# Optimization experiments

Hardware: AMD Instinct MI355X
Metric: run time of the kernel (lower is better)

## Reference

```python
import jax, jax.numpy as jnp
import numpy as np

N = 50000
E = 800000
D_IN = 128
D_OUT = 128
LN_EPS = 1e-5
NEG_SLOPE = 0.01  # torch LeakyReLU default


def setup_inputs() -> dict:
    key = jax.random.key(0)
    ks = jax.random.split(key, 6)
    x = jax.random.normal(ks[0], (N, D_IN), dtype=jnp.float32)
    edgeIndex = jax.random.randint(ks[1], (2, E), 0, N, dtype=jnp.int64)
    edgeAttribute = jax.random.uniform(ks[2], (E,), dtype=jnp.float32)
    ln_w = jnp.ones((D_IN,), jnp.float32)
    ln_b = jnp.zeros((D_IN,), jnp.float32)
    W_gcn = jax.random.normal(ks[3], (D_IN, D_OUT), dtype=jnp.float32) / np.sqrt(D_IN)
    b_gcn = jnp.zeros((D_OUT,), jnp.float32)
    W_lin = jax.random.normal(ks[4], (D_IN, D_OUT), dtype=jnp.float32) / np.sqrt(D_IN)
    b_lin = jnp.zeros((D_OUT,), jnp.float32)
    return dict(x=x, edgeIndex=edgeIndex, edgeAttribute=edgeAttribute,
                ln_w=ln_w, ln_b=ln_b, W_gcn=W_gcn, b_gcn=b_gcn,
                W_lin=W_lin, b_lin=b_lin)


def _layernorm(x, w, b):
    mu = jnp.mean(x, axis=-1, keepdims=True)
    var = jnp.mean(jnp.square(x - mu), axis=-1, keepdims=True)
    return (x - mu) * jax.lax.rsqrt(var + LN_EPS) * w + b


def _gcn_conv(x, edge_index, edge_weight, W, b):
    # PyG GCNConv: h = X W; add self-loops (w=1); D^-1/2 (A+I) D^-1/2 h + b
    n = x.shape[0]
    h = x @ W  # [N, D_OUT]
    loop = jnp.arange(n, dtype=edge_index.dtype)
    row = jnp.concatenate([edge_index[0], loop])  # source j
    col = jnp.concatenate([edge_index[1], loop])  # target i
    ew = jnp.concatenate([edge_weight, jnp.ones((n,), edge_weight.dtype)])
    deg = jax.ops.segment_sum(ew, col, num_segments=n)  # in-degree (weighted)
    dinv = jnp.where(deg > 0, jax.lax.rsqrt(deg), 0.0)
    norm = dinv[row] * ew * dinv[col]  # [E+N]
    msg = h[row] * norm[:, None]  # gather-scale, [E+N, D_OUT]
    out = jax.ops.segment_sum(msg, col, num_segments=n)  # scatter-add
    return out + b


def reference(x, edgeIndex, edgeAttribute, ln_w, ln_b, W_gcn, b_gcn, W_lin, b_lin):
    xn = _layernorm(x, ln_w, ln_b)
    g = _gcn_conv(xn, edgeIndex, edgeAttribute, W_gcn, b_gcn)
    x_out = jnp.where(g >= 0, g, NEG_SLOPE * g)  # LeakyReLU; dropout in eval = identity
    x_trans = xn @ W_lin + b_lin
    return x_out + x_trans
```

## Files before the change

kernel.cpp:

```cpp
#include <hip/hip_runtime.h>
#include <hip/hip_bf16.h>

#define DD 128
#define LN_EPS_ 1e-5f
#define SLOPE 0.01f
#define SB 128
#define NB 391
#define HB 64
#define LNB 12500

typedef __attribute__((ext_vector_type(8))) short bf16x8;
typedef __attribute__((ext_vector_type(4))) float f32x4;
typedef __attribute__((ext_vector_type(2))) float f32x2;
typedef __attribute__((ext_vector_type(2))) unsigned int u32x2;

__device__ __forceinline__ __hip_bfloat162 pack_bf162(float a, float b) {
  __hip_bfloat162 r;
  r.x = __float2bfloat16(a);
  r.y = __float2bfloat16(b);
  return r;
}

__device__ __forceinline__ float b2f(short v) {
  return __uint_as_float(((unsigned)(unsigned short)v) << 16);
}

__device__ __forceinline__ unsigned short f2bbits(float f) {
  __hip_bfloat16 h = __float2bfloat16(f);
  return *(unsigned short*)&h;
}


__launch_bounds__(256)
__global__ void k_big1(const int* __restrict__ eic, int* __restrict__ bhistT,
                       int* __restrict__ bcurOff,
                       const float* __restrict__ x, const float* __restrict__ lnw,
                       const float* __restrict__ lnb, __hip_bfloat162* __restrict__ xnB,
                       const float* __restrict__ Wg, const float* __restrict__ Wl,
                       __hip_bfloat16* __restrict__ pw, int ne, int n) {
  __shared__ int lh[NB];
  int bid = blockIdx.x;
  int t = threadIdx.x;
  if (bid < HB) {
    for (int i = t; i < NB; i += 256) lh[i] = 0;
    __syncthreads();
    for (int e = bid * 256 + t; e < ne; e += HB * 256) atomicAdd(&lh[eic[e] >> 7], 1);
    __syncthreads();
    for (int i = t; i < NB; i += 256) bhistT[i * HB + bid] = lh[i];
    if (bid == 0)
      for (int i = t; i < NB; i += 256) bcurOff[i] = 0;
  } else if (bid < HB + LNB) {
    int lane = t & 63;
    int row = (bid - HB) * 4 + (t >> 6);
    if (row >= n) return;
    float2 v = ((const float2*)(x + (size_t)row * DD))[lane];
    float s = v.x + v.y;
#pragma unroll
    for (int m = 32; m; m >>= 1) s += __shfl_xor(s, m, 64);
    float mu = s * 0.0078125f;
    float ex = v.x - mu, ey = v.y - mu;
    float q = ex * ex + ey * ey;
#pragma unroll
    for (int m = 32; m; m >>= 1) q += __shfl_xor(q, m, 64);
    float rstd = rsqrtf(q * 0.0078125f + LN_EPS_);
    float2 wv = ((const float2*)lnw)[lane];
    float2 bv = ((const float2*)lnb)[lane];
    xnB[(size_t)row * 64 + lane] =
        pack_bf162(ex * rstd * wv.x + bv.x, ey * rstd * wv.y + bv.y);
  } else {
    int idx = (bid - HB - LNB) * 256 + t;
    if (idx >= 2 * 16384) return;
    int j = idx & 7;
    int lane = (idx >> 3) & 63;
    int ks = (idx >> 9) & 3;
    int ct = (idx >> 11) & 7;
    int mat = idx >> 14;
    int col = ct * 16 + (lane & 15);
    int k = ks * 32 + (lane >> 4) * 8 + j;
    const float* W = mat ? Wl : Wg;
    pw[idx] = __float2bfloat16(W[k * DD + col]);
  }
}


__launch_bounds__(512)
__global__ void k_scatterA(const int* __restrict__ ei, const float* __restrict__ ew,
                           const int* __restrict__ bhistT, int* __restrict__ bcurOff,
                           int* __restrict__ bbase, uint2* __restrict__ packA, int ne) {
  __shared__ int lhist[NB];
  __shared__ int lbase[NB];
  __shared__ int sc[2][512];
  int t = threadIdx.x;

  int v = 0;
  if (t < NB) {
    const int4* col = (const int4*)(bhistT + t * HB);
#pragma unroll
    for (int b = 0; b < HB / 4; ++b) {
      int4 c = col[b];
      v += c.x + c.y + c.z + c.w;
    }
  }
  sc[0][t] = v;
  __syncthreads();
  int pb = 0;
  for (int off = 1; off < 512; off <<= 1) {
    sc[pb ^ 1][t] = sc[pb][t] + (t >= off ? sc[pb][t - off] : 0);
    pb ^= 1;
    __syncthreads();
  }
  int inc = sc[pb][t];
  if (t < NB) {
    lbase[t] = inc - v;
    lhist[t] = 0;
  }
  if (blockIdx.x == 0) {
    if (t < NB) bbase[t] = inc - v;
    if (t == NB - 1) bbase[NB] = inc;
  }
  __syncthreads();

  int per = (ne + gridDim.x - 1) / gridDim.x;
  int e0 = blockIdx.x * per, e1 = min(ne, e0 + per);
  for (int e = e0 + t; e < e1; e += 512) atomicAdd(&lhist[ei[ne + e] >> 7], 1);
  __syncthreads();
  if (t < NB) {
    int c = lhist[t];
    int off = c ? atomicAdd(&bcurOff[t], c) : 0;
    lbase[t] += off;
    lhist[t] = 0;
  }
  __syncthreads();
  for (int e = e0 + t; e < e1; e += 512) {
    int c = ei[ne + e];
    int sb = c >> 7, tl = c & 127;
    int p = lbase[sb] + atomicAdd(&lhist[sb], 1);
    packA[p] = make_uint2((unsigned)ei[e] | ((unsigned)tl << 16), __float_as_uint(ew[e]));
  }
}


__launch_bounds__(256)
__global__ void k_csr(const uint2* __restrict__ packA, const int* __restrict__ bbase,
                      unsigned* __restrict__ packB, int* __restrict__ baseG,
                      int* __restrict__ cntG, float* __restrict__ dinv,
                      const __hip_bfloat162* __restrict__ xnB,
                      unsigned char* __restrict__ ynF8, int n) {
  __shared__ int cnt[SB];
  __shared__ float degl[SB];
  __shared__ int cur[SB];
  __shared__ int sc[2][SB];
  __shared__ float sdi[SB];
  int b = blockIdx.x;
  int t = threadIdx.x;
  if (t < SB) { cnt[t] = 0; degl[t] = 0.f; }
  __syncthreads();
  int eb = bbase[b], ee = bbase[b + 1];
  for (int e = eb + t; e < ee; e += 256) {
    uint2 pk = packA[e];
    int tl = (pk.x >> 16) & 0xFF;
    atomicAdd(&cnt[tl], 1);
    atomicAdd(&degl[tl], __uint_as_float(pk.y));
  }
  __syncthreads();
  if (t < SB) sc[0][t] = cnt[t];
  __syncthreads();
  int pb = 0;
  for (int off = 1; off < SB; off <<= 1) {
    if (t < SB) sc[pb ^ 1][t] = sc[pb][t] + (t >= off ? sc[pb][t - off] : 0);
    pb ^= 1;
    __syncthreads();
  }
  if (t < SB) {
    int node = b * SB + t;
    if (node < n) {
      int inc = sc[pb][t];
      int ex = inc - cnt[t];
      float di = rsqrtf(1.0f + degl[t]);
      dinv[node] = di;
      sdi[t] = di;
      baseG[node] = eb + ex;
      cntG[node] = cnt[t];
      cur[t] = ex;
    }
  }
  __syncthreads();
  {
    int nrow = min(SB, n - b * SB);
    for (int idx = t; idx < nrow * 32; idx += 256) {
      int r = idx >> 5, c = idx & 31;
      int node = b * SB + r;
      float di = sdi[r];
      float2 v0 = __bfloat1622float2(xnB[(size_t)node * 64 + c * 2]);
      float2 v1 = __bfloat1622float2(xnB[(size_t)node * 64 + c * 2 + 1]);
      int wbits = __builtin_amdgcn_cvt_pk_fp8_f32(v0.x * di, v0.y * di, 0, false);
      wbits = __builtin_amdgcn_cvt_pk_fp8_f32(v1.x * di, v1.y * di, wbits, true);
      ((int*)ynF8)[(size_t)node * 32 + c] = wbits;
    }
  }
  for (int e = eb + t; e < ee; e += 256) {
    uint2 pk = packA[e];
    int tl = (pk.x >> 16) & 0xFF;
    int p = atomicAdd(&cur[tl], 1);
    packB[eb + p] = ((pk.x & 0xFFFFu) << 16) | (unsigned)f2bbits(__uint_as_float(pk.y));
  }
}


__launch_bounds__(256)
__global__ void k_gf(const unsigned* __restrict__ packB, const int* __restrict__ base,
                     const int* __restrict__ cnt, const __hip_bfloat162* __restrict__ xnB,
                     const unsigned char* __restrict__ ynF8,
                     const float* __restrict__ dinv, const short* __restrict__ pw,
                     const float* __restrict__ bg, const float* __restrict__ bl,
                     float* __restrict__ out, int n) {
  __shared__ short tile[16][136];
  int t = threadIdx.x;
  int lane = t & 63, w = t >> 6;
  int g = lane >> 4;
  int sub = lane & 15;
  int row0 = blockIdx.x * 16;
  const short* xnS = (const short*)xnB;
  int i0 = row0 + w * 4;

  int baseN[4], dcN[4];
  float diN[4];
#pragma unroll
  for (int nd = 0; nd < 4; ++nd) {
    baseN[nd] = base[i0 + nd];
    dcN[nd] = cnt[i0 + nd];
    diN[nd] = dinv[i0 + nd];
  }

  float s8[4][8];
#pragma unroll
  for (int nd = 0; nd < 4; ++nd)
#pragma unroll
    for (int j = 0; j < 8; ++j) s8[nd][j] = 0.f;

#pragma unroll
  for (int nd = 0; nd < 4; ++nd) {
    if (g == 0) {
      bf16x8 xi = *(const bf16x8*)(xnS + (size_t)(i0 + nd) * DD + sub * 8);
#pragma unroll
      for (int j = 0; j < 8; ++j) s8[nd][j] = b2f(xi[j]) * diN[nd];
    }
  }

  int dcmax = max(max(dcN[0], dcN[1]), max(dcN[2], dcN[3]));
  for (int eb = 0; eb < dcmax; eb += 64) {
    unsigned pkN[4];
#pragma unroll
    for (int nd = 0; nd < 4; ++nd)
      pkN[nd] = (eb + lane < dcN[nd]) ? packB[baseN[nd] + eb + lane] : 0u;
    int mm = min(64, dcmax - eb);
    for (int j0 = 0; j0 < mm; j0 += 8) {
#pragma unroll
      for (int nd = 0; nd < 4; ++nd) {
        unsigned ca = (unsigned)__shfl((int)pkN[nd], j0 + g, 64);
        unsigned cb = (unsigned)__shfl((int)pkN[nd], j0 + g + 4, 64);
        int sa = ca >> 16, sb = cb >> 16;
        float wa = b2f((short)(ca & 0xFFFFu));
        float wb = b2f((short)(cb & 0xFFFFu));
        u32x2 ra = *(const u32x2*)(ynF8 + (size_t)sa * DD + sub * 8);
        u32x2 rb = *(const u32x2*)(ynF8 + (size_t)sb * DD + sub * 8);
        f32x2 a0 = __builtin_amdgcn_cvt_pk_f32_fp8(ra[0], false);
        f32x2 a1 = __builtin_amdgcn_cvt_pk_f32_fp8(ra[0], true);
        f32x2 a2 = __builtin_amdgcn_cvt_pk_f32_fp8(ra[1], false);
        f32x2 a3 = __builtin_amdgcn_cvt_pk_f32_fp8(ra[1], true);
        s8[nd][0] = fmaf(a0[0], wa, s8[nd][0]);
        s8[nd][1] = fmaf(a0[1], wa, s8[nd][1]);
        s8[nd][2] = fmaf(a1[0], wa, s8[nd][2]);
        s8[nd][3] = fmaf(a1[1], wa, s8[nd][3]);
        s8[nd][4] = fmaf(a2[0], wa, s8[nd][4]);
        s8[nd][5] = fmaf(a2[1], wa, s8[nd][5]);
        s8[nd][6] = fmaf(a3[0], wa, s8[nd][6]);
        s8[nd][7] = fmaf(a3[1], wa, s8[nd][7]);
        f32x2 b0 = __builtin_amdgcn_cvt_pk_f32_fp8(rb[0], false);
        f32x2 b1 = __builtin_amdgcn_cvt_pk_f32_fp8(rb[0], true);
        f32x2 b2 = __builtin_amdgcn_cvt_pk_f32_fp8(rb[1], false);
        f32x2 b3 = __builtin_amdgcn_cvt_pk_f32_fp8(rb[1], true);
        s8[nd][0] = fmaf(b0[0], wb, s8[nd][0]);
        s8[nd][1] = fmaf(b0[1], wb, s8[nd][1]);
        s8[nd][2] = fmaf(b1[0], wb, s8[nd][2]);
        s8[nd][3] = fmaf(b1[1], wb, s8[nd][3]);
        s8[nd][4] = fmaf(b2[0], wb, s8[nd][4]);
        s8[nd][5] = fmaf(b2[1], wb, s8[nd][5]);
        s8[nd][6] = fmaf(b3[0], wb, s8[nd][6]);
        s8[nd][7] = fmaf(b3[1], wb, s8[nd][7]);
      }
    }
  }

#pragma unroll
  for (int nd = 0; nd < 4; ++nd) {
#pragma unroll
    for (int j = 0; j < 8; ++j) {
      s8[nd][j] += __shfl_xor(s8[nd][j], 16, 64);
      s8[nd][j] += __shfl_xor(s8[nd][j], 32, 64);
      s8[nd][j] *= diN[nd];
    }
    if (g == 0) {
      bf16x8 o;
#pragma unroll
      for (int j = 0; j < 4; ++j) {
        __hip_bfloat162 p2 = pack_bf162(s8[nd][2 * j], s8[nd][2 * j + 1]);
        o[2 * j] = *(short*)&p2.x;
        o[2 * j + 1] = *(short*)&p2.y;
      }
      *(bf16x8*)&tile[w * 4 + nd][sub * 8] = o;
    }
  }
  __syncthreads();

  bf16x8 ag[4], al[4];
#pragma unroll
  for (int ks = 0; ks < 4; ++ks) {
    ag[ks] = *(const bf16x8*)(&tile[sub][g * 8] + ks * 32);
    al[ks] = *(const bf16x8*)(xnS + (size_t)(row0 + sub) * DD + g * 8 + ks * 32);
  }

#pragma unroll
  for (int cc = 0; cc < 2; ++cc) {
    int ct = w * 2 + cc;
    f32x4 cg = {0.f, 0.f, 0.f, 0.f}, cl = {0.f, 0.f, 0.f, 0.f};
#pragma unroll
    for (int ks = 0; ks < 4; ++ks) {
      bf16x8 bgf = *(const bf16x8*)(pw + ((size_t)(0 * 8 + ct) * 4 + ks) * 512 + lane * 8);
      bf16x8 blf = *(const bf16x8*)(pw + ((size_t)(1 * 8 + ct) * 4 + ks) * 512 + lane * 8);
      cg = __builtin_amdgcn_mfma_f32_16x16x32_bf16(ag[ks], bgf, cg, 0, 0, 0);
      cl = __builtin_amdgcn_mfma_f32_16x16x32_bf16(al[ks], blf, cl, 0, 0, 0);
    }
    int colg = ct * 16 + sub;
    float bgv = bg[colg], blv = bl[colg];
#pragma unroll
    for (int r = 0; r < 4; ++r) {
      int row = row0 + g * 4 + r;
      float gg = cg[r] + bgv;
      gg = (gg >= 0.f) ? gg : SLOPE * gg;
      out[(size_t)row * DD + colg] = gg + cl[r] + blv;
    }
  }
}

extern "C" void kernel_launch(void* const* d_in, const int* in_sizes, int n_in,
                              void* d_out, int out_size, void* d_ws, size_t ws_size,
                              hipStream_t stream) {
  const float* x   = (const float*)d_in[0];
  const int*   ei  = (const int*)d_in[1];
  const float* ew  = (const float*)d_in[2];
  const float* lnw = (const float*)d_in[3];
  const float* lnb = (const float*)d_in[4];
  const float* Wg  = (const float*)d_in[5];
  const float* bg  = (const float*)d_in[6];
  const float* Wl  = (const float*)d_in[7];
  const float* bl  = (const float*)d_in[8];
  float* out = (float*)d_out;

  int n  = in_sizes[0] / DD;
  int ne = in_sizes[1] / 2;

  uint2* packA = (uint2*)d_ws;
  unsigned* packB = (unsigned*)(packA + ne);
  __hip_bfloat162* xnB = (__hip_bfloat162*)(packB + ne);
  unsigned char* ynF8 = (unsigned char*)(xnB + (size_t)n * 64);
  __hip_bfloat16* pw = (__hip_bfloat16*)(ynF8 + (size_t)n * DD);
  float* dinv = (float*)(pw + 32768);
  int* base   = (int*)(dinv + n);
  int* cnt    = base + n;
  int* bhistT = cnt + n;
  int* bbase  = bhistT + NB * HB;
  int* bcurOff= bbase + NB + 1;

  int packBlocks = (2 * 16384 + 255) / 256;
  k_big1<<<HB + LNB + packBlocks, 256, 0, stream>>>(ei + ne, bhistT, bcurOff,
                                                    x, lnw, lnb, xnB, Wg, Wl, pw, ne, n);
  k_scatterA<<<200, 512, 0, stream>>>(ei, ew, bhistT, bcurOff, bbase, packA, ne);
  k_csr<<<NB, 256, 0, stream>>>(packA, bbase, packB, base, cnt, dinv, xnB, ynF8, n);
  k_gf<<<(n + 15) / 16, 256, 0, stream>>>(packB, base, cnt, xnB, ynF8, dinv,
                                          (const short*)pw, bg, bl, out, n);
}
```

Before: 99.70 us.

## Fuse CSR build and gather-MFMA into one kernel with LDS edge list

Merges the CSR-construction kernel and the gather/GEMM kernel into a single 391-block kernel. Each block sorts its bucket's edges into shared memory and then aggregates and runs the MFMA projections for 128 rows, so the packB and base/count arrays no longer make a round trip through global memory. Degree is now accumulated with global float atomics in the scatter pass. The source-side normalization moves from an fp8 pre-scaled feature table into the per-edge weight, so LayerNorm writes unscaled fp8 directly. The trade-offs are far fewer blocks (391 instead of about 3125), which lowers parallelism for the gather phase. Edges per bucket are also capped at 3072, so a bucket with more edges is silently truncated, and the fp8 quantization now happens before the dinv scaling.

Measured after the change: 130.4 us. +30.8%, slower.

```diff
diff --git a/kernel.cpp b/kernel.cpp
--- a/kernel.cpp
+++ b/kernel.cpp
@@ -8,6 +8,7 @@
 #define NB 391
 #define HB 64
 #define LNB 12500
+#define CAPE 3072
 
 typedef __attribute__((ext_vector_type(8))) short bf16x8;
 typedef __attribute__((ext_vector_type(4))) float f32x4;
@@ -36,6 +37,7 @@
                        int* __restrict__ bcurOff,
                        const float* __restrict__ x, const float* __restrict__ lnw,
                        const float* __restrict__ lnb, __hip_bfloat162* __restrict__ xnB,
+                       unsigned char* __restrict__ xnF8, float* __restrict__ deg,
                        const float* __restrict__ Wg, const float* __restrict__ Wl,
                        __hip_bfloat16* __restrict__ pw, int ne, int n) {
   __shared__ int lh[NB];
@@ -65,8 +67,12 @@
     float rstd = rsqrtf(q * 0.0078125f + LN_EPS_);
     float2 wv = ((const float2*)lnw)[lane];
     float2 bv = ((const float2*)lnb)[lane];
-    xnB[(size_t)row * 64 + lane] =
-        pack_bf162(ex * rstd * wv.x + bv.x, ey * rstd * wv.y + bv.y);
+    float ox = ex * rstd * wv.x + bv.x;
+    float oy = ey * rstd * wv.y + bv.y;
+    xnB[(size_t)row * 64 + lane] = pack_bf162(ox, oy);
+    int wbits = __builtin_amdgcn_cvt_pk_fp8_f32(ox, oy, 0, false);
+    ((unsigned short*)xnF8)[(size_t)row * 64 + lane] = (unsigned short)(wbits & 0xFFFF);
+    if (lane == 0) deg[row] = 1.0f;
   } else {
     int idx = (bid - HB - LNB) * 256 + t;
     if (idx >= 2 * 16384) return;
@@ -86,7 +92,8 @@
 __launch_bounds__(512)
 __global__ void k_scatterA(const int* __restrict__ ei, const float* __restrict__ ew,
                            const int* __restrict__ bhistT, int* __restrict__ bcurOff,
-                           int* __restrict__ bbase, uint2* __restrict__ packA, int ne) {
+                           int* __restrict__ bbase, uint2* __restrict__ packA,
+                           float* __restrict__ deg, int ne) {
   __shared__ int lhist[NB];
   __shared__ int lbase[NB];
   __shared__ int sc[2][512];
@@ -122,7 +129,11 @@
 
   int per = (ne + gridDim.x - 1) / gridDim.x;
   int e0 = blockIdx.x * per, e1 = min(ne, e0 + per);
-  for (int e = e0 + t; e < e1; e += 512) atomicAdd(&lhist[ei[ne + e] >> 7], 1);
+  for (int e = e0 + t; e < e1; e += 512) {
+    int c = ei[ne + e];
+    atomicAdd(&lhist[c >> 7], 1);
+    unsafeAtomicAdd(&deg[c], ew[e]);
+  }
   __syncthreads();
   if (t < NB) {
     int c = lhist[t];
@@ -140,28 +151,33 @@
 }
 
 
-__launch_bounds__(256)
-__global__ void k_csr(const uint2* __restrict__ packA, const int* __restrict__ bbase,
-                      unsigned* __restrict__ packB, int* __restrict__ baseG,
-                      int* __restrict__ cntG, float* __restrict__ dinv,
-                      const __hip_bfloat162* __restrict__ xnB,
-                      unsigned char* __restrict__ ynF8, int n) {
-  __shared__ int cnt[SB];
-  __shared__ float degl[SB];
-  __shared__ int cur[SB];
+__launch_bounds__(512)
+__global__ void k_csrgf(const uint2* __restrict__ packA, const int* __restrict__ bbase,
+                        const float* __restrict__ deg,
+                        const __hip_bfloat162* __restrict__ xnB,
+                        const unsigned char* __restrict__ xnF8,
+                        const short* __restrict__ pw,
+                        const float* __restrict__ bg, const float* __restrict__ bl,
+                        float* __restrict__ out, int n) {
+  __shared__ unsigned ledge[CAPE];
+  __shared__ short tile[SB][136];
+  __shared__ int cnt[SB], cur[SB], nbase[SB];
+  __shared__ float sdi[SB];
   __shared__ int sc[2][SB];
-  __shared__ float sdi[SB];
   int b = blockIdx.x;
   int t = threadIdx.x;
-  if (t < SB) { cnt[t] = 0; degl[t] = 0.f; }
-  __syncthreads();
-  int eb = bbase[b], ee = bbase[b + 1];
-  for (int e = eb + t; e < ee; e += 256) {
-    uint2 pk = packA[e];
-    int tl = (pk.x >> 16) & 0xFF;
-    atomicAdd(&cnt[tl], 1);
-    atomicAdd(&degl[tl], __uint_as_float(pk.y));
-  }
+  int lane = t & 63, w = t >> 6;
+  int g = lane >> 4;
+  int sub = lane & 15;
+  int row0 = b * SB;
+  const short* xnS = (const short*)xnB;
+
+  int eb = bbase[b];
+  int ecnt = min(bbase[b + 1] - eb, CAPE);
+  if (t < SB) cnt[t] = 0;
+  __syncthreads();
+  for (int e = t; e < ecnt; e += 512)
+    atomicAdd(&cnt[(packA[eb + e].x >> 16) & 0xFF], 1);
   __syncthreads();
   if (t < SB) sc[0][t] = cnt[t];
   __syncthreads();
@@ -172,173 +188,140 @@
     __syncthreads();
   }
   if (t < SB) {
-    int node = b * SB + t;
-    if (node < n) {
-      int inc = sc[pb][t];
-      int ex = inc - cnt[t];
-      float di = rsqrtf(1.0f + degl[t]);
-      dinv[node] = di;
-      sdi[t] = di;
-      baseG[node] = eb + ex;
-      cntG[node] = cnt[t];
-      cur[t] = ex;
-    }
-  }
-  __syncthreads();
-  {
-    int nrow = min(SB, n - b * SB);
-    for (int idx = t; idx < nrow * 32; idx += 256) {
-      int r = idx >> 5, c = idx & 31;
-      int node = b * SB + r;
-      float di = sdi[r];
-      float2 v0 = __bfloat1622float2(xnB[(size_t)node * 64 + c * 2]);
-      float2 v1 = __bfloat1622float2(xnB[(size_t)node * 64 + c * 2 + 1]);
-      int wbits = __builtin_amdgcn_cvt_pk_fp8_f32(v0.x * di, v0.y * di, 0, false);
-      wbits = __builtin_amdgcn_cvt_pk_fp8_f32(v1.x * di, v1.y * di, wbits, true);
-      ((int*)ynF8)[(size_t)node * 32 + c] = wbits;
-    }
-  }
-  for (int e = eb + t; e < ee; e += 256) {
-    uint2 pk = packA[e];
+    int ex = sc[pb][t] - cnt[t];
+    nbase[t] = ex;
+    cur[t] = ex;
+    int node = row0 + t;
+    sdi[t] = (node < n) ? rsqrtf(deg[node]) : 0.f;
+  }
+  __syncthreads();
+  for (int e = t; e < ecnt; e += 512) {
+    uint2 pk = packA[eb + e];
     int tl = (pk.x >> 16) & 0xFF;
-    int p = atomicAdd(&cur[tl], 1);
-    packB[eb + p] = ((pk.x & 0xFFFFu) << 16) | (unsigned)f2bbits(__uint_as_float(pk.y));
-  }
-}
-
-
-__launch_bounds__(256)
-__global__ void k_gf(const unsigned* __restrict__ packB, const int* __restrict__ base,
-                     const int* __restrict__ cnt, const __hip_bfloat162* __restrict__ xnB,
-                     const unsigned char* __restrict__ ynF8,
-                     const float* __restrict__ dinv, const short* __restrict__ pw,
-                     const float* __restrict__ bg, const float* __restrict__ bl,
-                     float* __restrict__ out, int n) {
-  __shared__ short tile[16][136];
-  int t = threadIdx.x;
-  int lane = t & 63, w = t >> 6;
-  int g = lane >> 4;
-  int sub = lane & 15;
-  int row0 = blockIdx.x * 16;
-  const short* xnS = (const short*)xnB;
-  int i0 = row0 + w * 4;
-
-  int baseN[4], dcN[4];
-  float diN[4];
-#pragma unroll
-  for (int nd = 0; nd < 4; ++nd) {
-    baseN[nd] = base[i0 + nd];
-    dcN[nd] = cnt[i0 + nd];
-    diN[nd] = dinv[i0 + nd];
-  }
-
-  float s8[4][8];
-#pragma unroll
-  for (int nd = 0; nd < 4; ++nd)
-#pragma unroll
-    for (int j = 0; j < 8; ++j) s8[nd][j] = 0.f;
-
-#pragma unroll
-  for (int nd = 0; nd < 4; ++nd) {
-    if (g == 0) {
-      bf16x8 xi = *(const bf16x8*)(xnS + (size_t)(i0 + nd) * DD + sub * 8);
-#pragma unroll
-      for (int j = 0; j < 8; ++j) s8[nd][j] = b2f(xi[j]) * diN[nd];
-    }
-  }
-
-  int dcmax = max(max(dcN[0], dcN[1]), max(dcN[2], dcN[3]));
-  for (int eb = 0; eb < dcmax; eb += 64) {
-    unsigned pkN[4];
+    int src = pk.x & 0xFFFF;
+    float wgt = rsqrtf(deg[src]) * __uint_as_float(pk.y);
+    int pos = atomicAdd(&cur[tl], 1);
+    ledge[pos] = ((unsigned)src << 16) | (unsigned)f2bbits(wgt);
+  }
+  __syncthreads();
+
+  for (int rr = 0; rr < 4; ++rr) {
+    int l0 = w * 16 + rr * 4;
+    int baseN[4], dcN[4];
+    float diN[4];
+#pragma unroll
+    for (int nd = 0; nd < 4; ++nd) {
+      baseN[nd] = nbase[l0 + nd];
+      dcN[nd] = cnt[l0 + nd];
+      diN[nd] = sdi[l0 + nd];
+    }
+    float s8[4][8];
 #pragma unroll
     for (int nd = 0; nd < 4; ++nd)
-      pkN[nd] = (eb + lane < dcN[nd]) ? packB[baseN[nd] + eb + lane] : 0u;
-    int mm = min(64, dcmax - eb);
-    for (int j0 = 0; j0 < mm; j0 += 8) {
-#pragma unroll
-      for (int nd = 0; nd < 4; ++nd) {
-        unsigned ca = (unsigned)__shfl((int)pkN[nd], j0 + g, 64);
-        unsigned cb = (unsigned)__shfl((int)pkN[nd], j0 + g + 4, 64);
-        int sa = ca >> 16, sb = cb >> 16;
-        float wa = b2f((short)(ca & 0xFFFFu));
-        float wb = b2f((short)(cb & 0xFFFFu));
-        u32x2 ra = *(const u32x2*)(ynF8 + (size_t)sa * DD + sub * 8);
-        u32x2 rb = *(const u32x2*)(ynF8 + (size_t)sb * DD + sub * 8);
-        f32x2 a0 = __builtin_amdgcn_cvt_pk_f32_fp8(ra[0], false);
-        f32x2 a1 = __builtin_amdgcn_cvt_pk_f32_fp8(ra[0], true);
-        f32x2 a2 = __builtin_amdgcn_cvt_pk_f32_fp8(ra[1], false);
-        f32x2 a3 = __builtin_amdgcn_cvt_pk_f32_fp8(ra[1], true);
-        s8[nd][0] = fmaf(a0[0], wa, s8[nd][0]);
-        s8[nd][1] = fmaf(a0[1], wa, s8[nd][1]);
-        s8[nd][2] = fmaf(a1[0], wa, s8[nd][2]);
-        s8[nd][3] = fmaf(a1[1], wa, s8[nd][3]);
-        s8[nd][4] = fmaf(a2[0], wa, s8[nd][4]);
-        s8[nd][5] = fmaf(a2[1], wa, s8[nd][5]);
-        s8[nd][6] = fmaf(a3[0], wa, s8[nd][6]);
-        s8[nd][7] = fmaf(a3[1], wa, s8[nd][7]);
-        f32x2 b0 = __builtin_amdgcn_cvt_pk_f32_fp8(rb[0], false);
-        f32x2 b1 = __builtin_amdgcn_cvt_pk_f32_fp8(rb[0], true);
-        f32x2 b2 = __builtin_amdgcn_cvt_pk_f32_fp8(rb[1], false);
-        f32x2 b3 = __builtin_amdgcn_cvt_pk_f32_fp8(rb[1], true);
-        s8[nd][0] = fmaf(b0[0], wb, s8[nd][0]);
-        s8[nd][1] = fmaf(b0[1], wb, s8[nd][1]);
-        s8[nd][2] = fmaf(b1[0], wb, s8[nd][2]);
-        s8[nd][3] = fmaf(b1[1], wb, s8[nd][3]);
-        s8[nd][4] = fmaf(b2[0], wb, s8[nd][4]);
-        s8[nd][5] = fmaf(b2[1], wb, s8[nd][5]);
-        s8[nd][6] = fmaf(b3[0], wb, s8[nd][6]);
-        s8[nd][7] = fmaf(b3[1], wb, s8[nd][7]);
-      }
-    }
-  }
-
-#pragma unroll
-  for (int nd = 0; nd < 4; ++nd) {
-#pragma unroll
-    for (int j = 0; j < 8; ++j) {
-      s8[nd][j] += __shfl_xor(s8[nd][j], 16, 64);
-      s8[nd][j] += __shfl_xor(s8[nd][j], 32, 64);
-      s8[nd][j] *= diN[nd];
-    }
-    if (g == 0) {
-      bf16x8 o;
-#pragma unroll
-      for (int j = 0; j < 4; ++j) {
-        __hip_bfloat162 p2 = pack_bf162(s8[nd][2 * j], s8[nd][2 * j + 1]);
-        o[2 * j] = *(short*)&p2.x;
-        o[2 * j + 1] = *(short*)&p2.y;
-      }
-      *(bf16x8*)&tile[w * 4 + nd][sub * 8] = o;
-    }
-  }
-  __syncthreads();
-
-  bf16x8 ag[4], al[4];
+#pragma unroll
+      for (int j = 0; j < 8; ++j) s8[nd][j] = 0.f;
+#pragma unroll
+    for (int nd = 0; nd < 4; ++nd) {
+      int i = row0 + l0 + nd;
+      if (g == 0 && i < n) {
+        bf16x8 xi = *(const bf16x8*)(xnS + (size_t)i * DD + sub * 8);
+#pragma unroll
+        for (int j = 0; j < 8; ++j) s8[nd][j] = b2f(xi[j]) * diN[nd];
+      }
+    }
+    int dcmax = max(max(dcN[0], dcN[1]), max(dcN[2], dcN[3]));
+    for (int eb0 = 0; eb0 < dcmax; eb0 += 64) {
+      unsigned pkN[4];
+#pragma unroll
+      for (int nd = 0; nd < 4; ++nd)
+        pkN[nd] = (eb0 + lane < dcN[nd]) ? ledge[baseN[nd] + eb0 + lane] : 0u;
+      int mm = min(64, dcmax - eb0);
+      for (int j0 = 0; j0 < mm; j0 += 8) {
+#pragma unroll
+        for (int nd = 0; nd < 4; ++nd) {
+          unsigned ca = (unsigned)__shfl((int)pkN[nd], j0 + g, 64);
+          unsigned cb = (unsigned)__shfl((int)pkN[nd], j0 + g + 4, 64);
+          int sa = ca >> 16, sb = cb >> 16;
+          float wa = b2f((short)(ca & 0xFFFFu));
+          float wb = b2f((short)(cb & 0xFFFFu));
+          u32x2 ra = *(const u32x2*)(xnF8 + (size_t)sa * DD + sub * 8);
+          u32x2 rb = *(const u32x2*)(xnF8 + (size_t)sb * DD + sub * 8);
+          f32x2 a0 = __builtin_amdgcn_cvt_pk_f32_fp8(ra[0], false);
+          f32x2 a1 = __builtin_amdgcn_cvt_pk_f32_fp8(ra[0], true);
+          f32x2 a2 = __builtin_amdgcn_cvt_pk_f32_fp8(ra[1], false);
+          f32x2 a3 = __builtin_amdgcn_cvt_pk_f32_fp8(ra[1], true);
+          s8[nd][0] = fmaf(a0[0], wa, s8[nd][0]);
+          s8[nd][1] = fmaf(a0[1], wa, s8[nd][1]);
+          s8[nd][2] = fmaf(a1[0], wa, s8[nd][2]);
+          s8[nd][3] = fmaf(a1[1], wa, s8[nd][3]);
+          s8[nd][4] = fmaf(a2[0], wa, s8[nd][4]);
+          s8[nd][5] = fmaf(a2[1], wa, s8[nd][5]);
+          s8[nd][6] = fmaf(a3[0], wa, s8[nd][6]);
+          s8[nd][7] = fmaf(a3[1], wa, s8[nd][7]);
+          f32x2 b0 = __builtin_amdgcn_cvt_pk_f32_fp8(rb[0], false);
+          f32x2 b1 = __builtin_amdgcn_cvt_pk_f32_fp8(rb[0], true);
+          f32x2 b2 = __builtin_amdgcn_cvt_pk_f32_fp8(rb[1], false);
+          f32x2 b3 = __builtin_amdgcn_cvt_pk_f32_fp8(rb[1], true);
+          s8[nd][0] = fmaf(b0[0], wb, s8[nd][0]);
+          s8[nd][1] = fmaf(b0[1], wb, s8[nd][1]);
+          s8[nd][2] = fmaf(b1[0], wb, s8[nd][2]);
+          s8[nd][3] = fmaf(b1[1], wb, s8[nd][3]);
+          s8[nd][4] = fmaf(b2[0], wb, s8[nd][4]);
+          s8[nd][5] = fmaf(b2[1], wb, s8[nd][5]);
+          s8[nd][6] = fmaf(b3[0], wb, s8[nd][6]);
+          s8[nd][7] = fmaf(b3[1], wb, s8[nd][7]);
+        }
+      }
+    }
+#pragma unroll
+    for (int nd = 0; nd < 4; ++nd) {
+#pragma unroll
+      for (int j = 0; j < 8; ++j) {
+        s8[nd][j] += __shfl_xor(s8[nd][j], 16, 64);
+        s8[nd][j] += __shfl_xor(s8[nd][j], 32, 64);
+        s8[nd][j] *= diN[nd];
+      }
+      if (g == 0) {
+        bf16x8 o;
+#pragma unroll
+        for (int j = 0; j < 4; ++j) {
+          __hip_bfloat162 p2 = pack_bf162(s8[nd][2 * j], s8[nd][2 * j + 1]);
+          o[2 * j] = *(short*)&p2.x;
+          o[2 * j + 1] = *(short*)&p2.y;
+        }
+        *(bf16x8*)&tile[l0 + nd][sub * 8] = o;
+      }
+    }
+  }
+  __syncthreads();
+
+  int ct = w;
+  bf16x8 bgf[4], blf[4];
 #pragma unroll
   for (int ks = 0; ks < 4; ++ks) {
-    ag[ks] = *(const bf16x8*)(&tile[sub][g * 8] + ks * 32);
-    al[ks] = *(const bf16x8*)(xnS + (size_t)(row0 + sub) * DD + g * 8 + ks * 32);
-  }
-
-#pragma unroll
-  for (int cc = 0; cc < 2; ++cc) {
-    int ct = w * 2 + cc;
+    bgf[ks] = *(const bf16x8*)(pw + ((size_t)(0 * 8 + ct) * 4 + ks) * 512 + lane * 8);
+    blf[ks] = *(const bf16x8*)(pw + ((size_t)(1 * 8 + ct) * 4 + ks) * 512 + lane * 8);
+  }
+  int colg = ct * 16 + sub;
+  float bgv = bg[colg], blv = bl[colg];
+  for (int rt = 0; rt < 8; ++rt) {
+    int arow = min(row0 + rt * 16 + sub, n - 1);
     f32x4 cg = {0.f, 0.f, 0.f, 0.f}, cl = {0.f, 0.f, 0.f, 0.f};
 #pragma unroll
     for (int ks = 0; ks < 4; ++ks) {
-      bf16x8 bgf = *(const bf16x8*)(pw + ((size_t)(0 * 8 + ct) * 4 + ks) * 512 + lane * 8);
-      bf16x8 blf = *(const bf16x8*)(pw + ((size_t)(1 * 8 + ct) * 4 + ks) * 512 + lane * 8);
-      cg = __builtin_amdgcn_mfma_f32_16x16x32_bf16(ag[ks], bgf, cg, 0, 0, 0);
-      cl = __builtin_amdgcn_mfma_f32_16x16x32_bf16(al[ks], blf, cl, 0, 0, 0);
-    }
-    int colg = ct * 16 + sub;
-    float bgv = bg[colg], blv = bl[colg];
+      bf16x8 ag = *(const bf16x8*)(&tile[rt * 16 + sub][g * 8] + ks * 32);
+      bf16x8 al = *(const bf16x8*)(xnS + (size_t)arow * DD + g * 8 + ks * 32);
+      cg = __builtin_amdgcn_mfma_f32_16x16x32_bf16(ag, bgf[ks], cg, 0, 0, 0);
+      cl = __builtin_amdgcn_mfma_f32_16x16x32_bf16(al, blf[ks], cl, 0, 0, 0);
+    }
 #pragma unroll
     for (int r = 0; r < 4; ++r) {
-      int row = row0 + g * 4 + r;
-      float gg = cg[r] + bgv;
-      gg = (gg >= 0.f) ? gg : SLOPE * gg;
-      out[(size_t)row * DD + colg] = gg + cl[r] + blv;
+      int row = row0 + rt * 16 + g * 4 + r;
+      if (row < n) {
+        float gg = cg[r] + bgv;
+        gg = (gg >= 0.f) ? gg : SLOPE * gg;
+        out[(size_t)row * DD + colg] = gg + cl[r] + blv;
+      }
     }
   }
 }
@@ -361,22 +344,19 @@
   int ne = in_sizes[1] / 2;
 
   uint2* packA = (uint2*)d_ws;
-  unsigned* packB = (unsigned*)(packA + ne);
-  __hip_bfloat162* xnB = (__hip_bfloat162*)(packB + ne);
-  unsigned char* ynF8 = (unsigned char*)(xnB + (size_t)n * 64);
-  __hip_bfloat16* pw = (__hip_bfloat16*)(ynF8 + (size_t)n * DD);
-  float* dinv = (float*)(pw + 32768);
-  int* base   = (int*)(dinv + n);
-  int* cnt    = base + n;
-  int* bhistT = cnt + n;
+  __hip_bfloat162* xnB = (__hip_bfloat162*)(packA + ne);
+  unsigned char* xnF8 = (unsigned char*)(xnB + (size_t)n * 64);
+  __hip_bfloat16* pw = (__hip_bfloat16*)(xnF8 + (size_t)n * DD);
+  float* deg  = (float*)(pw + 32768);
+  int* bhistT = (int*)(deg + n);
   int* bbase  = bhistT + NB * HB;
   int* bcurOff= bbase + NB + 1;
 
   int packBlocks = (2 * 16384 + 255) / 256;
   k_big1<<<HB + LNB + packBlocks, 256, 0, stream>>>(ei + ne, bhistT, bcurOff,
-                                                    x, lnw, lnb, xnB, Wg, Wl, pw, ne, n);
-  k_scatterA<<<200, 512, 0, stream>>>(ei, ew, bhistT, bcurOff, bbase, packA, ne);
-  k_csr<<<NB, 256, 0, stream>>>(packA, bbase, packB, base, cnt, dinv, xnB, ynF8, n);
-  k_gf<<<(n + 15) / 16, 256, 0, stream>>>(packB, base, cnt, xnB, ynF8, dinv,
-                                          (const short*)pw, bg, bl, out, n);
-}
+                                                    x, lnw, lnb, xnB, xnF8, deg,
+                                                    Wg, Wl, pw, ne, n);
+  k_scatterA<<<200, 512, 0, stream>>>(ei, ew, bhistT, bcurOff, bbase, packA, deg, ne);
+  k_csrgf<<<NB, 512, 0, stream>>>(packA, bbase, deg, xnB, xnF8,
+                                  (const short*)pw, bg, bl, out, n);
+}
```

## Move LayerNorm and weight packing into the scatter kernel to overlap stages

Applied to the files above, without the earlier changes.

Splits the fused histogram/LayerNorm/weight-pack kernel so that only the small histogram runs first. The LayerNorm and weight-packing blocks move into the bucket-scatter kernel as extra 512-thread blocks, so that independent work can fill the GPU while the scatter blocks run. The aim is to shorten the critical path by hiding the scatter kernel's latency behind LayerNorm. The cost is a larger shared-memory footprint per block and changed occupancy for the LayerNorm blocks.

Measured after the change: 99.91 us. About the same (+0.2%).

```diff
diff --git a/kernel.cpp b/kernel.cpp
--- a/kernel.cpp
+++ b/kernel.cpp
@@ -7,7 +7,8 @@
 #define SB 128
 #define NB 391
 #define HB 64
-#define LNB 12500
+#define SCB 200
+#define LNB2 6250
 
 typedef __attribute__((ext_vector_type(8))) short bf16x8;
 typedef __attribute__((ext_vector_type(4))) float f32x4;
@@ -32,26 +33,83 @@
 
 
 __launch_bounds__(256)
-__global__ void k_big1(const int* __restrict__ eic, int* __restrict__ bhistT,
-                       int* __restrict__ bcurOff,
-                       const float* __restrict__ x, const float* __restrict__ lnw,
-                       const float* __restrict__ lnb, __hip_bfloat162* __restrict__ xnB,
-                       const float* __restrict__ Wg, const float* __restrict__ Wl,
-                       __hip_bfloat16* __restrict__ pw, int ne, int n) {
+__global__ void k_hist(const int* __restrict__ eic, int* __restrict__ bhistT,
+                       int* __restrict__ bcurOff, int ne) {
   __shared__ int lh[NB];
   int bid = blockIdx.x;
   int t = threadIdx.x;
-  if (bid < HB) {
-    for (int i = t; i < NB; i += 256) lh[i] = 0;
-    __syncthreads();
-    for (int e = bid * 256 + t; e < ne; e += HB * 256) atomicAdd(&lh[eic[e] >> 7], 1);
-    __syncthreads();
-    for (int i = t; i < NB; i += 256) bhistT[i * HB + bid] = lh[i];
-    if (bid == 0)
-      for (int i = t; i < NB; i += 256) bcurOff[i] = 0;
-  } else if (bid < HB + LNB) {
+  for (int i = t; i < NB; i += 256) lh[i] = 0;
+  __syncthreads();
+  for (int e = bid * 256 + t; e < ne; e += HB * 256) atomicAdd(&lh[eic[e] >> 7], 1);
+  __syncthreads();
+  for (int i = t; i < NB; i += 256) bhistT[i * HB + bid] = lh[i];
+  if (bid == 0)
+    for (int i = t; i < NB; i += 256) bcurOff[i] = 0;
+}
+
+
+__launch_bounds__(512)
+__global__ void k_mix(const int* __restrict__ ei, const float* __restrict__ ew,
+                      const int* __restrict__ bhistT, int* __restrict__ bcurOff,
+                      int* __restrict__ bbase, uint2* __restrict__ packA,
+                      const float* __restrict__ x, const float* __restrict__ lnw,
+                      const float* __restrict__ lnb, __hip_bfloat162* __restrict__ xnB,
+                      const float* __restrict__ Wg, const float* __restrict__ Wl,
+                      __hip_bfloat16* __restrict__ pw, int ne, int n) {
+  int bid = blockIdx.x;
+  int t = threadIdx.x;
+  if (bid < SCB) {
+    __shared__ int lhist[NB];
+    __shared__ int lbase[NB];
+    __shared__ int sc[2][512];
+    int v = 0;
+    if (t < NB) {
+      const int4* col = (const int4*)(bhistT + t * HB);
+#pragma unroll
+      for (int b = 0; b < HB / 4; ++b) {
+        int4 c = col[b];
+        v += c.x + c.y + c.z + c.w;
+      }
+    }
+    sc[0][t] = v;
+    __syncthreads();
+    int pb = 0;
+    for (int off = 1; off < 512; off <<= 1) {
+      sc[pb ^ 1][t] = sc[pb][t] + (t >= off ? sc[pb][t - off] : 0);
+      pb ^= 1;
+      __syncthreads();
+    }
+    int inc = sc[pb][t];
+    if (t < NB) {
+      lbase[t] = inc - v;
+      lhist[t] = 0;
+    }
+    if (bid == 0) {
+      if (t < NB) bbase[t] = inc - v;
+      if (t == NB - 1) bbase[NB] = inc;
+    }
+    __syncthreads();
+
+    int per = (ne + SCB - 1) / SCB;
+    int e0 = bid * per, e1 = min(ne, e0 + per);
+    for (int e = e0 + t; e < e1; e += 512) atomicAdd(&lhist[ei[ne + e] >> 7], 1);
+    __syncthreads();
+    if (t < NB) {
+      int c = lhist[t];
+      int off = c ? atomicAdd(&bcurOff[t], c) : 0;
+      lbase[t] += off;
+      lhist[t] = 0;
+    }
+    __syncthreads();
+    for (int e = e0 + t; e < e1; e += 512) {
+      int c = ei[ne + e];
+      int sb = c >> 7, tl = c & 127;
+      int p = lbase[sb] + atomicAdd(&lhist[sb], 1);
+      packA[p] = make_uint2((unsigned)ei[e] | ((unsigned)tl << 16), __float_as_uint(ew[e]));
+    }
+  } else if (bid < SCB + LNB2) {
     int lane = t & 63;
-    int row = (bid - HB) * 4 + (t >> 6);
+    int row = (bid - SCB) * 8 + (t >> 6);
     if (row >= n) return;
     float2 v = ((const float2*)(x + (size_t)row * DD))[lane];
     float s = v.x + v.y;
@@ -68,7 +126,7 @@
     xnB[(size_t)row * 64 + lane] =
         pack_bf162(ex * rstd * wv.x + bv.x, ey * rstd * wv.y + bv.y);
   } else {
-    int idx = (bid - HB - LNB) * 256 + t;
+    int idx = (bid - SCB - LNB2) * 512 + t;
     if (idx >= 2 * 16384) return;
     int j = idx & 7;
     int lane = (idx >> 3) & 63;
@@ -79,63 +137,6 @@
     int k = ks * 32 + (lane >> 4) * 8 + j;
     const float* W = mat ? Wl : Wg;
     pw[idx] = __float2bfloat16(W[k * DD + col]);
-  }
-}
-
-
-__launch_bounds__(512)
-__global__ void k_scatterA(const int* __restrict__ ei, const float* __restrict__ ew,
-                           const int* __restrict__ bhistT, int* __restrict__ bcurOff,
-                           int* __restrict__ bbase, uint2* __restrict__ packA, int ne) {
-  __shared__ int lhist[NB];
-  __shared__ int lbase[NB];
-  __shared__ int sc[2][512];
-  int t = threadIdx.x;
-
-  int v = 0;
-  if (t < NB) {
-    const int4* col = (const int4*)(bhistT + t * HB);
-#pragma unroll
-    for (int b = 0; b < HB / 4; ++b) {
-      int4 c = col[b];
-      v += c.x + c.y + c.z + c.w;
-    }
-  }
-  sc[0][t] = v;
-  __syncthreads();
-  int pb = 0;
-  for (int off = 1; off < 512; off <<= 1) {
-    sc[pb ^ 1][t] = sc[pb][t] + (t >= off ? sc[pb][t - off] : 0);
-    pb ^= 1;
-    __syncthreads();
-  }
-  int inc = sc[pb][t];
-  if (t < NB) {
-    lbase[t] = inc - v;
-    lhist[t] = 0;
-  }
-  if (blockIdx.x == 0) {
-    if (t < NB) bbase[t] = inc - v;
-    if (t == NB - 1) bbase[NB] = inc;
-  }
-  __syncthreads();
-
-  int per = (ne + gridDim.x - 1) / gridDim.x;
-  int e0 = blockIdx.x * per, e1 = min(ne, e0 + per);
-  for (int e = e0 + t; e < e1; e += 512) atomicAdd(&lhist[ei[ne + e] >> 7], 1);
-  __syncthreads();
-  if (t < NB) {
-    int c = lhist[t];
-    int off = c ? atomicAdd(&bcurOff[t], c) : 0;
-    lbase[t] += off;
-    lhist[t] = 0;
-  }
-  __syncthreads();
-  for (int e = e0 + t; e < e1; e += 512) {
-    int c = ei[ne + e];
-    int sb = c >> 7, tl = c & 127;
-    int p = lbase[sb] + atomicAdd(&lhist[sb], 1);
-    packA[p] = make_uint2((unsigned)ei[e] | ((unsigned)tl << 16), __float_as_uint(ew[e]));
   }
 }
 
@@ -372,10 +373,11 @@
   int* bbase  = bhistT + NB * HB;
   int* bcurOff= bbase + NB + 1;
 
-  int packBlocks = (2 * 16384 + 255) / 256;
-  k_big1<<<HB + LNB + packBlocks, 256, 0, stream>>>(ei + ne, bhistT, bcurOff,
-                                                    x, lnw, lnb, xnB, Wg, Wl, pw, ne, n);
-  k_scatterA<<<200, 512, 0, stream>>>(ei, ew, bhistT, bcurOff, bbase, packA, ne);
+  int pwBlocks = (2 * 16384 + 511) / 512;
+  k_hist<<<HB, 256, 0, stream>>>(ei + ne, bhistT, bcurOff, ne);
+  k_mix<<<SCB + LNB2 + pwBlocks, 512, 0, stream>>>(ei, ew, bhistT, bcurOff, bbase,
+                                                   packA, x, lnw, lnb, xnB,
+                                                   Wg, Wl, pw, ne, n);
   k_csr<<<NB, 256, 0, stream>>>(packA, bbase, packB, base, cnt, dinv, xnB, ynF8, n);
   k_gf<<<(n + 15) / 16, 256, 0, stream>>>(packB, base, cnt, xnB, ynF8, dinv,
                                           (const short*)pw, bg, bl, out, n);
```
